# Kernel tuning notes

Measured on AMD Instinct MI355X. Metric: run time of the kernel, lower is better.

## Reference

```python
import jax, jax.numpy as jnp
import numpy as np
from jax import lax

# Static config (matches init_kwargs / electrode montage)
B, T, V = 16, 1536, 64
F1, D, H = 16, 2, 4
F2 = F1 * D              # 32
FO = F2 // H             # 8, GAT per-head out dim
K1, K3 = 32, 16          # conv kernel sizes (temporal)
P1, P2 = 8, 4            # avg pool sizes
KNN = 4
EPS = 1e-5
NEG_SLOPE = 0.2          # PyG GATConv leaky_relu slope


def _build_edges():
    # deterministic electrode geometry -> kNN graph, plus PyG self-loops
    rng = np.random.RandomState(0)
    pos = rng.randn(V, 3)
    dmat = np.linalg.norm(pos[:, None] - pos[None, :], axis=-1)
    order = np.argsort(dmat, axis=1)
    nbrs = order[:, 1:KNN + 1]                      # exclude self
    src = np.repeat(np.arange(V), KNN)
    dst = nbrs.reshape(-1)
    # add self loops (GATConv default add_self_loops=True)
    src = np.concatenate([src, np.arange(V)])
    dst = np.concatenate([dst, np.arange(V)])
    return jnp.asarray(np.stack([src, dst]), dtype=jnp.int32)  # (2, E)


def _bn(x, g, b, m, v, axis):
    shp = [1] * x.ndim
    shp[axis] = -1
    rs = lambda a: a.reshape(shp)
    return rs(g) * (x - rs(m)) * lax.rsqrt(rs(v) + EPS) + rs(b)


def _conv_same_t(x, w, k):
    # Conv2d(..., (1,k), padding='same'): torch pads (k-1)//2 left, rest right
    lp = (k - 1) // 2
    return lax.conv_general_dilated(x, w, (1, 1), [(0, 0), (lp, k - 1 - lp)],
                                    dimension_numbers=('NCHW', 'OIHW', 'NCHW'))


def _gat(x, W, a_src, a_dst, bias, src, dst):
    # Batched PyG GATConv (eval mode, dropout off), concat heads.
    # x: (Ng, V, F1); W: (F1, H*FO); a_src/a_dst: (H, FO); bias: (H*FO,)
    Ng = x.shape[0]
    h = jnp.einsum('nvf,fho->nvho', x, W.reshape(F1, H, FO))   # (Ng,V,H,FO)
    es = jnp.einsum('nvho,ho->nvh', h, a_src)[:, src]          # (Ng,E,H)
    ed = jnp.einsum('nvho,ho->nvh', h, a_dst)[:, dst]
    e = jax.nn.leaky_relu(es + ed, NEG_SLOPE)
    # softmax over incoming edges of each target node (segment softmax)
    m = jnp.full((Ng, V, H), -1e30, e.dtype).at[:, dst].max(e)
    ex = jnp.exp(e - m[:, dst])
    den = jnp.zeros((Ng, V, H), e.dtype).at[:, dst].add(ex)
    alpha = ex / den[:, dst]                                   # (Ng,E,H)
    out = jnp.zeros((Ng, V, H, FO), e.dtype).at[:, dst].add(alpha[..., None] * h[:, src])
    return out.reshape(Ng, V, H * FO) + bias


def setup_inputs() -> dict:
    key = jax.random.key(0)
    ks = jax.random.split(key, 16)
    bn = lambda k, c: (1.0 + 0.1 * jax.random.normal(jax.random.fold_in(k, 0), (c,)),
                       0.1 * jax.random.normal(jax.random.fold_in(k, 1), (c,)),
                       0.1 * jax.random.normal(jax.random.fold_in(k, 2), (c,)),
                       0.5 + jax.random.uniform(jax.random.fold_in(k, 3), (c,)))
    bn1 = bn(ks[1], F1); bn2 = bn(ks[2], F2); bn3 = bn(ks[3], F2)
    inp = {
        'x': jax.random.normal(ks[0], (B, 1, V, T), jnp.float32),
        'conv1_w': 0.1 * jax.random.normal(ks[4], (F1, 1, 1, K1), jnp.float32),
        'bn1_g': bn1[0], 'bn1_b': bn1[1], 'bn1_m': bn1[2], 'bn1_v': bn1[3],
        'gat_w': (1.0 / np.sqrt(F1)) * jax.random.normal(ks[5], (F1, H * FO), jnp.float32),
        'gat_asrc': 0.3 * jax.random.normal(ks[6], (H, FO), jnp.float32),
        'gat_adst': 0.3 * jax.random.normal(ks[7], (H, FO), jnp.float32),
        'gat_bias': 0.05 * jax.random.normal(ks[8], (H * FO,), jnp.float32),
        'bn2_g': bn2[0], 'bn2_b': bn2[1], 'bn2_m': bn2[2], 'bn2_v': bn2[3],
        'conv3_w': 0.1 * jax.random.normal(ks[9], (F2, F2, 1, K3), jnp.float32),
        'bn3_g': bn3[0], 'bn3_b': bn3[1], 'bn3_m': bn3[2], 'bn3_v': bn3[3],
        'edge_index': _build_edges(),
    }
    return inp


def reference(x, conv1_w, bn1_g, bn1_b, bn1_m, bn1_v,
              gat_w, gat_asrc, gat_adst, gat_bias,
              bn2_g, bn2_b, bn2_m, bn2_v,
              conv3_w, bn3_g, bn3_b, bn3_m, bn3_v, edge_index):
    src, dst = edge_index[0], edge_index[1]
    # block1: temporal conv + BN
    h = _conv_same_t(x, conv1_w, K1)                 # (B,F1,V,T)
    h = _bn(h, bn1_g, bn1_b, bn1_m, bn1_v, 1)
    # spatial GNN over B*T independent electrode graphs
    xg = h.transpose(0, 3, 2, 1).reshape(B * T, V, F1)
    g = _gat(xg, gat_w, gat_asrc, gat_adst, gat_bias, src, dst)   # (BT,V,F2)
    g = g.mean(axis=1).reshape(B, T, F2).transpose(0, 2, 1)       # (B,F2,T)
    g = _bn(g, bn2_g, bn2_b, bn2_m, bn2_v, 1)[:, :, None, :]      # (B,F2,1,T)
    # tail: elu -> pool -> conv -> bn -> elu -> pool (dropout = eval no-op)
    h = jax.nn.elu(g)
    h = h.reshape(B, F2, 1, T // P1, P1).mean(-1)
    h = _conv_same_t(h, conv3_w, K3)
    h = _bn(h, bn3_g, bn3_b, bn3_m, bn3_v, 1)
    h = jax.nn.elu(h)
    h = h.reshape(B, F2, 1, T // P1 // P2, P2).mean(-1)           # (B,F2,1,48)
    return h
```

## Files before the change

kernel.cpp:

```cpp
#include <hip/hip_runtime.h>
#include <math.h>

#define TPB 256

constexpr int Bc = 16, Tc = 1536;
constexpr int T2c = 192;
constexpr float EPSc = 1e-5f;
constexpr float NSLOPE = 0.2f;
constexpr int MDI = 16;
constexpr int MDO = 8;

constexpr int OW_WEFF = 0;
constexpr int OW_CHL  = 1024;
constexpr int OW_A2   = 1056;
constexpr int OW_C2   = 1088;
constexpr int OW_A3   = 1120;
constexpr int OW_C3   = 1152;
constexpr int OW_WES  = 1184;
constexpr int OW_WED  = 1312;
constexpr int OW_CES  = 1440;
constexpr int OW_W3T  = 1448;
constexpr int OW_GRAPH= OW_W3T + 16384;
constexpr int OW_P    = OW_GRAPH + 512;

constexpr int GB_INTS = 417;

constexpr int L_XT  = 0;
constexpr int L_WBT = 2624;
constexpr int L_Y   = 4672;
constexpr int L_WE  = 5952;
constexpr int L_G   = 6208;
constexpr int L_GR  = 6464;
constexpr int L_TOT = 6884;

__global__ void prep_kernel(const float* __restrict__ c1w,
                            const float* __restrict__ g1, const float* __restrict__ b1,
                            const float* __restrict__ m1, const float* __restrict__ v1,
                            const float* __restrict__ W,  const float* __restrict__ bias,
                            const float* __restrict__ asrc, const float* __restrict__ adst,
                            const float* __restrict__ g2, const float* __restrict__ b2,
                            const float* __restrict__ m2, const float* __restrict__ v2,
                            const float* __restrict__ w3,
                            const float* __restrict__ g3, const float* __restrict__ b3,
                            const float* __restrict__ m3, const float* __restrict__ v3,
                            const int* __restrict__ ei, int ne, float* __restrict__ ws)
{
    const int tid = threadIdx.x;
    if (blockIdx.x > 0) {
        const int base = (blockIdx.x - 1) * 1024;
        for (int q = 0; q < 4; q++) {
            int idx = base + q * TPB + tid;
            int f2o = idx & 31, r = idx >> 5;
            int f2i = r & 31, k = r >> 5;
            ws[OW_W3T + idx] = w3[(f2o * 32 + f2i) * 16 + k];
        }
        return;
    }

    __shared__ float sweff[1024];
    __shared__ float schl[32];
    __shared__ int isrcp_i[64 * MDI];
    __shared__ int outdst_i[64 * MDO];
    __shared__ int indeg_i[64], inslot[64], outdeg_i[64], outslot[64];

    for (int idx = tid; idx < 1024; idx += TPB) {
        int k = idx >> 5, f2 = idx & 31;
        float s = 0.f;
        for (int f = 0; f < 16; f++) {
            float a1 = g1[f] * rsqrtf(v1[f] + EPSc);
            s += a1 * W[f * 32 + f2] * c1w[f * 32 + k];
        }
        ws[OW_WEFF + idx] = s;
        sweff[idx] = s;
    }
    for (int f2 = tid; f2 < 32; f2 += TPB) {
        float s = 0.f;
        for (int f = 0; f < 16; f++) {
            float a1 = g1[f] * rsqrtf(v1[f] + EPSc);
            float c1 = b1[f] - a1 * m1[f];
            s += c1 * W[f * 32 + f2];
        }
        ws[OW_CHL + f2] = s;
        schl[f2] = s;
        float a2 = g2[f2] * rsqrtf(v2[f2] + EPSc);
        ws[OW_A2 + f2] = a2;
        ws[OW_C2 + f2] = b2[f2] + a2 * (bias[f2] - m2[f2]);
        float a3 = g3[f2] * rsqrtf(v3[f2] + EPSc);
        ws[OW_A3 + f2] = a3;
        ws[OW_C3 + f2] = b3[f2] - a3 * m3[f2];
    }

    for (int i = tid; i < 64 * MDI; i += TPB) isrcp_i[i] = 0;
    for (int i = tid; i < 64 * MDO; i += TPB) outdst_i[i] = 0;
    if (tid < 64) { indeg_i[tid] = 0; inslot[tid] = 0; outdeg_i[tid] = 0; outslot[tid] = 0; }
    __syncthreads();
    for (int e = tid; e < ne; e += TPB) {
        atomicAdd(&indeg_i[ei[ne + e]], 1);
        atomicAdd(&outdeg_i[ei[e]], 1);
    }
    __syncthreads();
    for (int e = tid; e < ne; e += TPB) {
        int s = ei[e], d = ei[ne + e];
        int pi = atomicAdd(&inslot[d], 1);
        if (pi < MDI) isrcp_i[d * MDI + pi] = s;
        int po = atomicAdd(&outslot[s], 1);
        if (po < MDO) outdst_i[s * MDO + po] = d;
    }
    __syncthreads();
    if (tid < 128) {
        int k = tid >> 2, h = tid & 3;
        float s1 = 0.f, s2 = 0.f;
        for (int o = 0; o < 8; o++) {
            float wv = sweff[k * 32 + h * 8 + o];
            s1 = fmaf(asrc[h * 8 + o], wv, s1);
            s2 = fmaf(adst[h * 8 + o], wv, s2);
        }
        ws[OW_WES + tid] = s1;
        ws[OW_WED + tid] = s2;
    }
    if (tid < 4) {
        float s1 = 0.f, s2 = 0.f;
        for (int o = 0; o < 8; o++) {
            float cv = schl[tid * 8 + o];
            s1 = fmaf(asrc[tid * 8 + o], cv, s1);
            s2 = fmaf(adst[tid * 8 + o], cv, s2);
        }
        ws[OW_CES + tid] = s1;
        ws[OW_CES + 4 + tid] = s2;
    }
    unsigned char* gb = (unsigned char*)(ws + OW_GRAPH);
    for (int i = tid; i < 64 * MDI; i += TPB) gb[i] = (unsigned char)isrcp_i[i];
    for (int i = tid; i < 64; i += TPB) {
        gb[1024 + i] = (unsigned char)(indeg_i[i] < MDI ? indeg_i[i] : MDI);
        gb[1600 + i] = (unsigned char)(outdeg_i[i] < MDO ? outdeg_i[i] : MDO);
    }
    for (int i = tid; i < 64 * MDO; i += TPB) gb[1088 + i] = (unsigned char)outdst_i[i];
    if (tid == 0) {
        int mi = 0, mo = 0;
        for (int d = 0; d < 64; d++) {
            int a = indeg_i[d] < MDI ? indeg_i[d] : MDI;
            int b2_ = outdeg_i[d] < MDO ? outdeg_i[d] : MDO;
            mi = a > mi ? a : mi;
            mo = b2_ > mo ? b2_ : mo;
        }
        gb[1664] = (unsigned char)mi;
        gb[1665] = (unsigned char)mo;
    }
}

__global__ __launch_bounds__(TPB, 5) void gat_kernel(const float* __restrict__ x,
                                                     const float* __restrict__ wfp,
                                                     const float* __restrict__ chlp,
                                                     const float* __restrict__ wesed,
                                                     const float* __restrict__ cesed,
                                                     const float* __restrict__ a2p,
                                                     const float* __restrict__ c2p,
                                                     const int* __restrict__ graphi,
                                                     float* __restrict__ pout)
{
    __shared__ __align__(16) float sm[L_TOT];

    const int tid  = threadIdx.x;
    const int b    = blockIdx.x / 192;
    const int tile = blockIdx.x % 192;
    const int t0   = tile * 8;

    for (int idx = tid; idx < 64 * 41; idx += TPB) {
        int v = idx / 41, j = idx % 41;
        float val = 0.f;
        if (j < 39) {
            int t = t0 - 15 + j;
            val = (t >= 0 && t < Tc) ? x[(b * 64 + v) * Tc + t] : 0.f;
        } else if (j == 39) val = 1.0f;
        sm[L_XT + idx] = val;
    }
    sm[L_WE + tid] = wesed[tid];
    {
        int* gd = (int*)&sm[L_GR];
        for (int idx = tid; idx < GB_INTS; idx += TPB) gd[idx] = graphi[idx];
    }
    __syncthreads();

    const int wid = tid >> 6, v = tid & 63;
    const unsigned char* gb = (const unsigned char*)&sm[L_GR];

    float aes[8], aed[8];
    {
        const float cesh = cesed[wid], cedh = cesed[4 + wid];
        const float* xrow = &sm[L_XT + v * 41];
        #pragma unroll
        for (int t = 0; t < 8; t++) { aes[t] = cesh; aed[t] = cedh; }
        float xr[8];
        #pragma unroll
        for (int q = 0; q < 7; q++) xr[q] = xrow[q];
        #pragma unroll
        for (int k = 0; k < 32; k++) {
            xr[(k + 7) & 7] = xrow[k + 7];
            const float wek = sm[L_WE + k * 4 + wid];
            const float wdk = sm[L_WE + 128 + k * 4 + wid];
            #pragma unroll
            for (int t = 0; t < 8; t++) {
                const float xv = xr[(k + t) & 7];
                aes[t] = fmaf(xv, wek, aes[t]);
                aed[t] = fmaf(xv, wdk, aed[t]);
            }
        }
    }

    {
        const int indeg = gb[1024 + v];
        const int mdin  = gb[1664];
        float den[8] = { 0.f,0.f,0.f,0.f,0.f,0.f,0.f,0.f };
        for (int e = 0; e < mdin; e++) {
            const int s = gb[v * MDI + e];
            const float valid = (e < indeg) ? 1.f : 0.f;
            #pragma unroll
            for (int t = 0; t < 8; t++) {
                float ev = __shfl(aes[t], s) + aed[t];
                ev = ev > 0.f ? ev : NSLOPE * ev;
                den[t] += valid * __expf(ev);
            }
        }
        float rden[8];
        #pragma unroll
        for (int t = 0; t < 8; t++) rden[t] = 1.f / den[t];

        const int odeg = gb[1600 + v];
        const int mdo  = gb[1665];
        float wb[8] = { 0.f,0.f,0.f,0.f,0.f,0.f,0.f,0.f };
        for (int j = 0; j < mdo; j++) {
            const int d = gb[1088 + v * MDO + j];
            const float valid = (j < odeg) ? 1.f : 0.f;
            #pragma unroll
            for (int t = 0; t < 8; t++) {
                float ev = aes[t] + __shfl(aed[t], d);
                ev = ev > 0.f ? ev : NSLOPE * ev;
                wb[t] += valid * __expf(ev) * __shfl(rden[t], d);
            }
        }
        #pragma unroll
        for (int t = 0; t < 8; t++) sm[L_WBT + t * 256 + wid * 64 + v] = wb[t];
    }
    __syncthreads();

    if (tid < 160) {
        const int h = tid / 40, c = tid % 40;
        float ya[8] = { 0.f,0.f,0.f,0.f,0.f,0.f,0.f,0.f };
        #pragma unroll 4
        for (int v4 = 0; v4 < 16; v4++) {
            float xq[4];
            #pragma unroll
            for (int q = 0; q < 4; q++) xq[q] = sm[L_XT + (v4 * 4 + q) * 41 + c];
            #pragma unroll
            for (int t = 0; t < 8; t++) {
                const float4 w4 = *(const float4*)&sm[L_WBT + t * 256 + h * 64 + v4 * 4];
                ya[t] = fmaf(w4.x, xq[0], fmaf(w4.y, xq[1],
                        fmaf(w4.z, xq[2], fmaf(w4.w, xq[3], ya[t]))));
            }
        }
        #pragma unroll
        for (int t = 0; t < 8; t++) sm[L_Y + (t * 4 + h) * 40 + c] = ya[t];
    }
    __syncthreads();

    {
        const int t = tid >> 5, f2 = tid & 31, h = f2 >> 3;
        const float* yrow = &sm[L_Y + (t * 4 + h) * 40];
        float acc = chlp[f2] * yrow[39];
        #pragma unroll
        for (int k = 0; k < 32; k++)
            acc = fmaf(wfp[k * 32 + f2], yrow[t + k], acc);
        sm[L_G + t * 32 + f2] = acc;
    }
    __syncthreads();

    if (tid < 32) {
        const float a2l = a2p[tid], c2l = c2p[tid];
        float s = 0.f;
        #pragma unroll
        for (int t = 0; t < 8; t++) {
            float gv = sm[L_G + t * 32 + tid] * (1.f / 64.f);
            float y = fmaf(a2l, gv, c2l);
            s += y > 0.f ? y : __expf(y) - 1.f;
        }
        pout[(b * T2c + tile) * 32 + tid] = s * 0.125f;
    }
}

__global__ __launch_bounds__(TPB) void conv3_kernel(const float* __restrict__ pp,
                                                    const float* __restrict__ w3t,
                                                    const float* __restrict__ a3p,
                                                    const float* __restrict__ c3p,
                                                    float* __restrict__ outp)
{
    __shared__ float pl[63 * 32];
    __shared__ float q[48 * 32];
    const int tid = threadIdx.x;
    const int b = blockIdx.x >> 2, cc = blockIdx.x & 3;

    for (int idx = tid; idx < 63 * 32; idx += TPB) {
        int r = idx >> 5, f2 = idx & 31;
        int tog = cc * 48 - 7 + r;
        pl[idx] = (tog >= 0 && tog < T2c) ? pp[(b * T2c + tog) * 32 + f2] : 0.f;
    }
    __syncthreads();

    const int f2o = tid & 31, grp = tid >> 5;
    const int tb = grp * 6;
    float acc[6] = { 0.f, 0.f, 0.f, 0.f, 0.f, 0.f };
    for (int f2i = 0; f2i < 32; f2i++) {
        float seg[21];
        #pragma unroll
        for (int r = 0; r < 21; r++) seg[r] = pl[(tb + r) * 32 + f2i];
        #pragma unroll
        for (int k = 0; k < 16; k++) {
            float wv = w3t[(k * 32 + f2i) * 32 + f2o];
            #pragma unroll
            for (int j = 0; j < 6; j++)
                acc[j] = fmaf(seg[j + k], wv, acc[j]);
        }
    }
    const float a3 = a3p[f2o], c3 = c3p[f2o];
    #pragma unroll
    for (int j = 0; j < 6; j++) {
        float y = fmaf(a3, acc[j], c3);
        y = y > 0.f ? y : __expf(y) - 1.f;
        q[(tb + j) * 32 + f2o] = y;
    }
    __syncthreads();
    for (int idx = tid; idx < 12 * 32; idx += TPB) {
        int t4 = idx >> 5, f2 = idx & 31;
        int r0 = t4 * 4;
        float s = q[r0 * 32 + f2] + q[(r0 + 1) * 32 + f2] +
                  q[(r0 + 2) * 32 + f2] + q[(r0 + 3) * 32 + f2];
        outp[(b * 32 + f2) * 48 + cc * 12 + t4] = s * 0.25f;
    }
}

extern "C" void kernel_launch(void* const* d_in, const int* in_sizes, int n_in,
                              void* d_out, int out_size, void* d_ws, size_t ws_size,
                              hipStream_t stream)
{
    const float* x    = (const float*)d_in[0];
    const float* c1w  = (const float*)d_in[1];
    const float* g1   = (const float*)d_in[2];
    const float* b1   = (const float*)d_in[3];
    const float* m1   = (const float*)d_in[4];
    const float* v1   = (const float*)d_in[5];
    const float* W    = (const float*)d_in[6];
    const float* asrc = (const float*)d_in[7];
    const float* adst = (const float*)d_in[8];
    const float* bias = (const float*)d_in[9];
    const float* g2   = (const float*)d_in[10];
    const float* b2   = (const float*)d_in[11];
    const float* m2   = (const float*)d_in[12];
    const float* v2   = (const float*)d_in[13];
    const float* w3   = (const float*)d_in[14];
    const float* g3   = (const float*)d_in[15];
    const float* b3   = (const float*)d_in[16];
    const float* m3   = (const float*)d_in[17];
    const float* v3   = (const float*)d_in[18];
    const int*   ei   = (const int*)d_in[19];
    const int    ne   = in_sizes[19] / 2;

    float* ws = (float*)d_ws;

    prep_kernel<<<17, TPB, 0, stream>>>(c1w, g1, b1, m1, v1, W, bias, asrc, adst,
                                        g2, b2, m2, v2, w3, g3, b3, m3, v3, ei, ne, ws);

    gat_kernel<<<Bc * T2c, TPB, 0, stream>>>(x,
                                             ws + OW_WEFF, ws + OW_CHL,
                                             ws + OW_WES, ws + OW_CES,
                                             ws + OW_A2, ws + OW_C2,
                                             (const int*)(ws + OW_GRAPH),
                                             ws + OW_P);

    conv3_kernel<<<Bc * 4, TPB, 0, stream>>>(ws + OW_P, ws + OW_W3T,
                                             ws + OW_A3, ws + OW_C3, (float*)d_out);
}
```

Baseline: 184.3 us.

## Make GAT aggregation per-wavefront, drop block barriers, fold conv3 weight prep into conv3

The GAT kernel now gives each wavefront one head. It computes that head's weighted aggregation and filter outputs from its own LDS region and uses s_waitcnt instead of __syncthreads, removing two block-wide barriers. The Weff and chl filters are staged into LDS, and the 160-thread aggregation step becomes an all-thread layout with padded strides. conv3 now transposes w3 into a padded LDS copy and computes its BN constants inline, so prep runs as one block and skips a separate degree-counting pass. The risk is that cross-lane LDS visibility within a wavefront depends on lockstep execution, and every conv3 block repeats a 64 KB weight load.

```diff
diff --git a/kernel.cpp b/kernel.cpp
--- a/kernel.cpp
+++ b/kernel.cpp
@@ -14,24 +14,22 @@
 constexpr int OW_CHL  = 1024;
 constexpr int OW_A2   = 1056;
 constexpr int OW_C2   = 1088;
-constexpr int OW_A3   = 1120;
-constexpr int OW_C3   = 1152;
 constexpr int OW_WES  = 1184;
-constexpr int OW_WED  = 1312;
 constexpr int OW_CES  = 1440;
-constexpr int OW_W3T  = 1448;
-constexpr int OW_GRAPH= OW_W3T + 16384;
-constexpr int OW_P    = OW_GRAPH + 512;
+constexpr int OW_GRAPH= 1448;
+constexpr int OW_P    = 1872;
 
 constexpr int GB_INTS = 417;
 
 constexpr int L_XT  = 0;
-constexpr int L_WBT = 2624;
-constexpr int L_Y   = 4672;
-constexpr int L_WE  = 5952;
-constexpr int L_G   = 6208;
-constexpr int L_GR  = 6464;
-constexpr int L_TOT = 6884;
+constexpr int L_WF  = 2624;
+constexpr int L_WE  = 3648;
+constexpr int L_WB  = 3904;
+constexpr int L_Y   = 5984;
+constexpr int L_G   = 7296;
+constexpr int L_CHL = 7552;
+constexpr int L_GR  = 7584;
+constexpr int L_TOT = 8001;
 
 __global__ void prep_kernel(const float* __restrict__ c1w,
                             const float* __restrict__ g1, const float* __restrict__ b1,
@@ -40,28 +38,14 @@
                             const float* __restrict__ asrc, const float* __restrict__ adst,
                             const float* __restrict__ g2, const float* __restrict__ b2,
                             const float* __restrict__ m2, const float* __restrict__ v2,
-                            const float* __restrict__ w3,
-                            const float* __restrict__ g3, const float* __restrict__ b3,
-                            const float* __restrict__ m3, const float* __restrict__ v3,
                             const int* __restrict__ ei, int ne, float* __restrict__ ws)
 {
     const int tid = threadIdx.x;
-    if (blockIdx.x > 0) {
-        const int base = (blockIdx.x - 1) * 1024;
-        for (int q = 0; q < 4; q++) {
-            int idx = base + q * TPB + tid;
-            int f2o = idx & 31, r = idx >> 5;
-            int f2i = r & 31, k = r >> 5;
-            ws[OW_W3T + idx] = w3[(f2o * 32 + f2i) * 16 + k];
-        }
-        return;
-    }
-
     __shared__ float sweff[1024];
     __shared__ float schl[32];
     __shared__ int isrcp_i[64 * MDI];
     __shared__ int outdst_i[64 * MDO];
-    __shared__ int indeg_i[64], inslot[64], outdeg_i[64], outslot[64];
+    __shared__ int inslot[64], outslot[64];
 
     for (int idx = tid; idx < 1024; idx += TPB) {
         int k = idx >> 5, f2 = idx & 31;
@@ -85,19 +69,11 @@
         float a2 = g2[f2] * rsqrtf(v2[f2] + EPSc);
         ws[OW_A2 + f2] = a2;
         ws[OW_C2 + f2] = b2[f2] + a2 * (bias[f2] - m2[f2]);
-        float a3 = g3[f2] * rsqrtf(v3[f2] + EPSc);
-        ws[OW_A3 + f2] = a3;
-        ws[OW_C3 + f2] = b3[f2] - a3 * m3[f2];
     }
 
     for (int i = tid; i < 64 * MDI; i += TPB) isrcp_i[i] = 0;
     for (int i = tid; i < 64 * MDO; i += TPB) outdst_i[i] = 0;
-    if (tid < 64) { indeg_i[tid] = 0; inslot[tid] = 0; outdeg_i[tid] = 0; outslot[tid] = 0; }
-    __syncthreads();
-    for (int e = tid; e < ne; e += TPB) {
-        atomicAdd(&indeg_i[ei[ne + e]], 1);
-        atomicAdd(&outdeg_i[ei[e]], 1);
-    }
+    if (tid < 64) { inslot[tid] = 0; outslot[tid] = 0; }
     __syncthreads();
     for (int e = tid; e < ne; e += TPB) {
         int s = ei[e], d = ei[ne + e];
@@ -116,7 +92,7 @@
             s2 = fmaf(adst[h * 8 + o], wv, s2);
         }
         ws[OW_WES + tid] = s1;
-        ws[OW_WED + tid] = s2;
+        ws[OW_WES + 128 + tid] = s2;
     }
     if (tid < 4) {
         float s1 = 0.f, s2 = 0.f;
@@ -130,18 +106,18 @@
     }
     unsigned char* gb = (unsigned char*)(ws + OW_GRAPH);
     for (int i = tid; i < 64 * MDI; i += TPB) gb[i] = (unsigned char)isrcp_i[i];
-    for (int i = tid; i < 64; i += TPB) {
-        gb[1024 + i] = (unsigned char)(indeg_i[i] < MDI ? indeg_i[i] : MDI);
-        gb[1600 + i] = (unsigned char)(outdeg_i[i] < MDO ? outdeg_i[i] : MDO);
-    }
     for (int i = tid; i < 64 * MDO; i += TPB) gb[1088 + i] = (unsigned char)outdst_i[i];
+    if (tid < 64) {
+        gb[1024 + tid] = (unsigned char)(inslot[tid] < MDI ? inslot[tid] : MDI);
+        gb[1600 + tid] = (unsigned char)(outslot[tid] < MDO ? outslot[tid] : MDO);
+    }
+    __syncthreads();
     if (tid == 0) {
         int mi = 0, mo = 0;
         for (int d = 0; d < 64; d++) {
-            int a = indeg_i[d] < MDI ? indeg_i[d] : MDI;
-            int b2_ = outdeg_i[d] < MDO ? outdeg_i[d] : MDO;
+            int a = gb[1024 + d], o = gb[1600 + d];
             mi = a > mi ? a : mi;
-            mo = b2_ > mo ? b2_ : mo;
+            mo = o > mo ? o : mo;
         }
         gb[1664] = (unsigned char)mi;
         gb[1665] = (unsigned char)mo;
@@ -174,19 +150,21 @@
         } else if (j == 39) val = 1.0f;
         sm[L_XT + idx] = val;
     }
+    for (int idx = tid; idx < 1024; idx += TPB) sm[L_WF + idx] = wfp[idx];
     sm[L_WE + tid] = wesed[tid];
+    if (tid < 32) sm[L_CHL + tid] = chlp[tid];
     {
         int* gd = (int*)&sm[L_GR];
         for (int idx = tid; idx < GB_INTS; idx += TPB) gd[idx] = graphi[idx];
     }
     __syncthreads();
 
-    const int wid = tid >> 6, v = tid & 63;
+    const int h = tid >> 6, v = tid & 63;
     const unsigned char* gb = (const unsigned char*)&sm[L_GR];
 
     float aes[8], aed[8];
     {
-        const float cesh = cesed[wid], cedh = cesed[4 + wid];
+        const float cesh = cesed[h], cedh = cesed[4 + h];
         const float* xrow = &sm[L_XT + v * 41];
         #pragma unroll
         for (int t = 0; t < 8; t++) { aes[t] = cesh; aed[t] = cedh; }
@@ -196,8 +174,8 @@
         #pragma unroll
         for (int k = 0; k < 32; k++) {
             xr[(k + 7) & 7] = xrow[k + 7];
-            const float wek = sm[L_WE + k * 4 + wid];
-            const float wdk = sm[L_WE + 128 + k * 4 + wid];
+            const float wek = sm[L_WE + k * 4 + h];
+            const float wdk = sm[L_WE + 128 + k * 4 + h];
             #pragma unroll
             for (int t = 0; t < 8; t++) {
                 const float xv = xr[(k + t) & 7];
@@ -239,37 +217,34 @@
             }
         }
         #pragma unroll
-        for (int t = 0; t < 8; t++) sm[L_WBT + t * 256 + wid * 64 + v] = wb[t];
-    }
-    __syncthreads();
-
-    if (tid < 160) {
-        const int h = tid / 40, c = tid % 40;
-        float ya[8] = { 0.f,0.f,0.f,0.f,0.f,0.f,0.f,0.f };
-        #pragma unroll 4
-        for (int v4 = 0; v4 < 16; v4++) {
-            float xq[4];
-            #pragma unroll
-            for (int q = 0; q < 4; q++) xq[q] = sm[L_XT + (v4 * 4 + q) * 41 + c];
-            #pragma unroll
-            for (int t = 0; t < 8; t++) {
-                const float4 w4 = *(const float4*)&sm[L_WBT + t * 256 + h * 64 + v4 * 4];
-                ya[t] = fmaf(w4.x, xq[0], fmaf(w4.y, xq[1],
-                        fmaf(w4.z, xq[2], fmaf(w4.w, xq[3], ya[t]))));
-            }
-        }
-        #pragma unroll
-        for (int t = 0; t < 8; t++) sm[L_Y + (t * 4 + h) * 40 + c] = ya[t];
-    }
-    __syncthreads();
-
-    {
-        const int t = tid >> 5, f2 = tid & 31, h = f2 >> 3;
-        const float* yrow = &sm[L_Y + (t * 4 + h) * 40];
-        float acc = chlp[f2] * yrow[39];
+        for (int t = 0; t < 8; t++) sm[L_WB + h * 520 + t * 65 + v] = wb[t];
+    }
+    __asm__ volatile("s_waitcnt lgkmcnt(0)" ::: "memory");
+
+    {
+        const int t = v >> 3, cg = v & 7;
+        const float* wbrow = &sm[L_WB + h * 520 + t * 65];
+        float ya[5] = { 0.f, 0.f, 0.f, 0.f, 0.f };
+        for (int vv = 0; vv < 64; vv++) {
+            const float wbv = wbrow[vv];
+            const float* xv = &sm[L_XT + vv * 41 + cg];
+            #pragma unroll
+            for (int q = 0; q < 5; q++)
+                ya[q] = fmaf(wbv, xv[q * 8], ya[q]);
+        }
+        float* yrow = &sm[L_Y + h * 328 + t * 41];
+        #pragma unroll
+        for (int q = 0; q < 5; q++) yrow[cg + q * 8] = ya[q];
+    }
+    __asm__ volatile("s_waitcnt lgkmcnt(0)" ::: "memory");
+
+    {
+        const int t = v >> 3, o = v & 7, f2 = h * 8 + o;
+        const float* yrow = &sm[L_Y + h * 328 + t * 41];
+        float acc = sm[L_CHL + f2] * yrow[39];
         #pragma unroll
         for (int k = 0; k < 32; k++)
-            acc = fmaf(wfp[k * 32 + f2], yrow[t + k], acc);
+            acc = fmaf(sm[L_WF + k * 32 + f2], yrow[t + k], acc);
         sm[L_G + t * 32 + f2] = acc;
     }
     __syncthreads();
@@ -288,16 +263,27 @@
 }
 
 __global__ __launch_bounds__(TPB) void conv3_kernel(const float* __restrict__ pp,
-                                                    const float* __restrict__ w3t,
-                                                    const float* __restrict__ a3p,
-                                                    const float* __restrict__ c3p,
+                                                    const float* __restrict__ w3,
+                                                    const float* __restrict__ g3,
+                                                    const float* __restrict__ b3,
+                                                    const float* __restrict__ m3,
+                                                    const float* __restrict__ v3,
                                                     float* __restrict__ outp)
 {
+    __shared__ float w3s[16 * 1057];
     __shared__ float pl[63 * 32];
     __shared__ float q[48 * 32];
     const int tid = threadIdx.x;
     const int b = blockIdx.x >> 2, cc = blockIdx.x & 3;
 
+    for (int idx4 = tid; idx4 < 4096; idx4 += TPB) {
+        const float4 w4 = *(const float4*)(w3 + idx4 * 4);
+        const int k0 = (idx4 * 4) & 15, f2i = (idx4 >> 2) & 31, f2o = idx4 >> 7;
+        const float wq[4] = { w4.x, w4.y, w4.z, w4.w };
+        #pragma unroll
+        for (int j = 0; j < 4; j++)
+            w3s[(k0 + j) * 1057 + f2i * 33 + f2o] = wq[j];
+    }
     for (int idx = tid; idx < 63 * 32; idx += TPB) {
         int r = idx >> 5, f2 = idx & 31;
         int tog = cc * 48 - 7 + r;
@@ -314,13 +300,14 @@
         for (int r = 0; r < 21; r++) seg[r] = pl[(tb + r) * 32 + f2i];
         #pragma unroll
         for (int k = 0; k < 16; k++) {
-            float wv = w3t[(k * 32 + f2i) * 32 + f2o];
+            float wv = w3s[k * 1057 + f2i * 33 + f2o];
             #pragma unroll
             for (int j = 0; j < 6; j++)
                 acc[j] = fmaf(seg[j + k], wv, acc[j]);
         }
     }
-    const float a3 = a3p[f2o], c3 = c3p[f2o];
+    const float a3 = g3[f2o] * rsqrtf(v3[f2o] + EPSc);
+    const float c3 = b3[f2o] - a3 * m3[f2o];
     #pragma unroll
     for (int j = 0; j < 6; j++) {
         float y = fmaf(a3, acc[j], c3);
@@ -365,8 +352,8 @@
 
     float* ws = (float*)d_ws;
 
-    prep_kernel<<<17, TPB, 0, stream>>>(c1w, g1, b1, m1, v1, W, bias, asrc, adst,
-                                        g2, b2, m2, v2, w3, g3, b3, m3, v3, ei, ne, ws);
+    prep_kernel<<<1, TPB, 0, stream>>>(c1w, g1, b1, m1, v1, W, bias, asrc, adst,
+                                       g2, b2, m2, v2, ei, ne, ws);
 
     gat_kernel<<<Bc * T2c, TPB, 0, stream>>>(x,
                                              ws + OW_WEFF, ws + OW_CHL,
@@ -375,6 +362,6 @@
                                              (const int*)(ws + OW_GRAPH),
                                              ws + OW_P);
 
-    conv3_kernel<<<Bc * 4, TPB, 0, stream>>>(ws + OW_P, ws + OW_W3T,
-                                             ws + OW_A3, ws + OW_C3, (float*)d_out);
+    conv3_kernel<<<Bc * 4, TPB, 0, stream>>>(ws + OW_P, w3, g3, b3, m3, v3,
+                                             (float*)d_out);
 }
```

Measured after the change: 179.2 us. -2.8%, faster.
